# Optimization experiments

Measured on AMD Instinct MI355X. Metric: run time of the kernel, lower is better.

Reference implementation:

```python
import jax, jax.numpy as jnp
import numpy as np
from jax import lax

THRESHOLD = 10.0  # p-norm threshold in HSEM
BN_EPS = 1e-5
DN = ('NCHW', 'OIHW', 'NCHW')


def setup_inputs() -> dict:
    key = jax.random.key(0)
    ks = jax.random.split(key, 9)
    b, c, h, w = 2, 256, 64, 64
    c_out = 512
    # scale x so pairwise L2 distances straddle the threshold (dense-ish hypergraph)
    x = jax.random.normal(ks[0], (b, c, h, w), dtype=jnp.float32) * 0.4
    fc_w = jax.random.normal(ks[1], (c, c), dtype=jnp.float32) * 0.02
    fc_b = jax.random.normal(ks[2], (c,), dtype=jnp.float32) * 0.02
    bn_gamma = jnp.ones((c,), dtype=jnp.float32)
    bn_beta = jnp.zeros((c,), dtype=jnp.float32)
    down_w = jax.random.normal(ks[3], (c, c, 3, 3), dtype=jnp.float32) * 0.02
    down_b = jax.random.normal(ks[4], (c,), dtype=jnp.float32) * 0.02
    out_w = jax.random.normal(ks[5], (c_out, c, 1, 1), dtype=jnp.float32) * 0.02
    out_b = jax.random.normal(ks[6], (c_out,), dtype=jnp.float32) * 0.02
    return {"x": x, "fc_w": fc_w, "fc_b": fc_b, "bn_gamma": bn_gamma,
            "bn_beta": bn_beta, "down_w": down_w, "down_b": down_b,
            "out_w": out_w, "out_b": out_b}


def _mean_agg(path, X):
    # path: [b, n_tgt, n_src], X: [b, n_src, d]; mean aggregation with inf->0 masking
    s = jnp.sum(path, axis=2, keepdims=True)           # [b, n_tgt, 1]
    norm = jnp.where(s > 0, 1.0 / jnp.where(s > 0, s, 1.0), 0.0)
    return norm * jnp.matmul(path, X)


def reference(x, fc_w, fc_b, bn_gamma, bn_beta, down_w, down_b, out_w, out_b):
    b, c, h, w = x.shape
    n = h * w
    xf = x.reshape(b, c, n).transpose(0, 2, 1)          # [b, n, c]
    # cdist (euclidean): ||a-b|| via expansion
    sq = jnp.sum(xf * xf, axis=-1)                      # [b, n]
    d2 = sq[:, :, None] + sq[:, None, :] - 2.0 * jnp.einsum('bnc,bmc->bnm', xf, xf)
    dist = jnp.sqrt(jnp.maximum(d2, 0.0))               # [b, n, n]
    hg = (dist < THRESHOLD).astype(x.dtype)             # dynamic hypergraph incidence
    # HyPConv: fc -> v2e (H^T) -> e2v (H)
    y = jnp.einsum('bnc,dc->bnd', xf, fc_w) + fc_b      # Linear(c1, c2)
    E = _mean_agg(jnp.swapaxes(hg, 1, 2), y)            # vertex -> edge
    v = _mean_agg(hg, E)                                # edge -> vertex
    xf = v + xf                                         # residual
    x4 = xf.transpose(0, 2, 1).reshape(b, c, h, w)
    # BatchNorm2d (training-mode batch statistics, biased var)
    mean = jnp.mean(x4, axis=(0, 2, 3))
    var = jnp.var(x4, axis=(0, 2, 3))
    xn = (x4 - mean[None, :, None, None]) * lax.rsqrt(var + BN_EPS)[None, :, None, None]
    xn = xn * bn_gamma[None, :, None, None] + bn_beta[None, :, None, None]
    xa = xn * jax.nn.sigmoid(xn)                        # SiLU
    # Downsample: pad (right=1, bottom=1) then 3x3 stride-2 VALID conv
    xp = jnp.pad(xa, ((0, 0), (0, 0), (0, 1), (0, 1)))
    xd = lax.conv_general_dilated(xp, down_w, (2, 2), 'VALID', dimension_numbers=DN)
    xd = xd + down_b[None, :, None, None]
    out = lax.conv_general_dilated(xd, out_w, (1, 1), 'VALID', dimension_numbers=DN)
    out = out + out_b[None, :, None, None]
    return out
```

## Files before the change

### kernel.cpp

```cpp
#include <hip/hip_runtime.h>
#include <hip/hip_bf16.h>
#include <math.h>

#define NPIX 4096
#define CH   256

#define OFF_XP    0u
#define OFF_XR    1048576u
#define OFF_VB    2097152u
#define OFF_TBS   3145728u
#define OFF_TBS2  4194304u
#define OFF_HG    5242880u
#define OFF_SQ    6291456u
#define OFF_PART  6299648u
#define OFF_BNSS  6365184u
#define OFF_DINV  6365696u
#define OFF_W3P   6373888u
#define OFF_WFCP  6668800u
#define OFF_WOUTP 6701568u

typedef __attribute__((ext_vector_type(8))) short bf16x8;
typedef __attribute__((ext_vector_type(16))) float f32x16;

static __device__ __forceinline__ short f2b(float f) {
  __hip_bfloat16 h = __float2bfloat16(f);
  return *reinterpret_cast<short*>(&h);
}
static __device__ __forceinline__ float b2f(short s) {
  union { unsigned u; float f; } r;
  r.u = ((unsigned)(unsigned short)s) << 16;
  return r.f;
}

static __device__ __forceinline__ bf16x8 byte2bf(unsigned byte) {
  union { unsigned u[4]; bf16x8 h; } r;
  r.u[0] = ((byte * 0x8001u) & 0x10001u) * 0x3F80u;
  r.u[1] = (((byte >> 2) * 0x8001u) & 0x10001u) * 0x3F80u;
  r.u[2] = (((byte >> 4) * 0x8001u) & 0x10001u) * 0x3F80u;
  r.u[3] = (((byte >> 6) * 0x8001u) & 0x10001u) * 0x3F80u;
  return r.h;
}

static __device__ __forceinline__ size_t packoff(int m, int c) {
  return ((size_t)((m >> 5) * 16 + (c >> 4)) * 2 + ((c >> 3) & 1)) * 256 + (m & 31) * 8 + (c & 7);
}

__global__ __launch_bounds__(256) void k_front(const float* __restrict__ x,
                                               short* __restrict__ xp,
                                               float* __restrict__ sq) {
  __shared__ float lds[256][33];
  __shared__ float red2[8][32];
  const int b = blockIdx.y;
  const int n0 = blockIdx.x * 32;
  const int t = threadIdx.x;
  const float* xb = x + (size_t)b * CH * NPIX + n0;
  const int j = t & 31, cg8 = t >> 5;
#pragma unroll 4
  for (int it = 0; it < 32; ++it) {
    const int c = it * 8 + cg8;
    lds[c][j] = xb[(size_t)c * NPIX + j];
  }
  __syncthreads();
  {
    const int n = t & 31, cg = t >> 5;
    float s = 0.f;
#pragma unroll 8
    for (int i = 0; i < 32; ++i) {
      const float v = lds[cg * 32 + i][n];
      s += v * v;
    }
    red2[cg][n] = s;
  }
  short* xpb = xp + (size_t)b * NPIX * CH;
#pragma unroll
  for (int i = 0; i < 4; ++i) {
    const int f = i * 256 + t;
    const int n = f & 31, c0 = (f >> 5) * 8;
    short tmp[8];
#pragma unroll
    for (int k = 0; k < 8; ++k) tmp[k] = f2b(lds[c0 + k][n]);
    short* dst = xpb + packoff(n0 + n, c0);
    *(short4*)dst = *(short4*)&tmp[0];
    *(short4*)(dst + 4) = *(short4*)&tmp[4];
  }
  __syncthreads();
  if (t < 32) {
    float s = 0.f;
#pragma unroll
    for (int cg = 0; cg < 8; ++cg) s += red2[cg][t];
    sq[b * NPIX + n0 + t] = s;
  }
}

__global__ void k_packall(const float* __restrict__ fc_w, const float* __restrict__ ow,
                          const float* __restrict__ dw, short* __restrict__ wfcp,
                          short* __restrict__ woutp, short* __restrict__ w3p) {
  const int i = blockIdx.x * 256 + threadIdx.x;
  if (i < 65536) {
    wfcp[packoff(i >> 8, i & 255)] = f2b(fc_w[i]);
  } else if (i < 196608) {
    const int j = i - 65536;
    woutp[packoff(j >> 8, j & 255)] = f2b(ow[j]);
  } else {
    const int j = i - 196608;
    const int oc = j / 2304;
    const int rem = j % 2304;
    const int c = rem / 9, tap = rem % 9;
    const size_t off = ((size_t)((tap * 8 + (oc >> 5)) * 16 + (c >> 4)) * 2 + ((c >> 3) & 1)) * 256
                     + (oc & 31) * 8 + (c & 7);
    w3p[off] = f2b(dw[j]);
  }
}

__global__ __launch_bounds__(256, 2) void k_gram3(const short* __restrict__ xp,
                                                  const float* __restrict__ sq,
                                                  unsigned* __restrict__ hgbit) {
  const int b = blockIdx.z;
  int tt = blockIdx.x;
  int bi = 0;
  while (true) { const int cnt = 16 - (bi >> 1); if (tt < cnt) break; tt -= cnt; ++bi; }
  const int bj = (bi >> 1) + tt;
  const int i0 = bi * 128, j0 = bj * 256;

  const int t = threadIdx.x;
  const int lane = t & 63, wid = t >> 6;
  const int wm = wid >> 1, wn = wid & 1;
  const int c = lane & 31, h = lane >> 5;
  const short* xb = xp + (size_t)b * NPIX * CH;
  const int ibase = i0 + wm * 64;
  const int jbase = j0 + wn * 128;

  f32x16 acc[2][4];
#pragma unroll
  for (int m = 0; m < 2; ++m)
#pragma unroll
    for (int n = 0; n < 4; ++n)
#pragma unroll
      for (int r = 0; r < 16; ++r) acc[m][n][r] = 0.f;

  const short* pa = xb + (size_t)(ibase >> 5) * 8192 + lane * 8;
  const short* pb = xb + (size_t)(jbase >> 5) * 8192 + lane * 8;

#pragma unroll 2
  for (int kb = 0; kb < 16; ++kb) {
    const bf16x8 a0 = *(const bf16x8*)(pa + kb * 512);
    const bf16x8 a1 = *(const bf16x8*)(pa + 8192 + kb * 512);
    bf16x8 bb[4];
#pragma unroll
    for (int n = 0; n < 4; ++n) bb[n] = *(const bf16x8*)(pb + (size_t)n * 8192 + kb * 512);
#pragma unroll
    for (int n = 0; n < 4; ++n) {
      acc[0][n] = __builtin_amdgcn_mfma_f32_32x32x16_bf16(a0, bb[n], acc[0][n], 0, 0, 0);
      acc[1][n] = __builtin_amdgcn_mfma_f32_32x32x16_bf16(a1, bb[n], acc[1][n], 0, 0, 0);
    }
  }

  const int sqb = b * NPIX;
#pragma unroll
  for (int m = 0; m < 2; ++m) {
    float4 sqa[4];
#pragma unroll
    for (int q = 0; q < 4; ++q)
      sqa[q] = *(const float4*)(sq + sqb + ibase + m * 32 + q * 8 + 4 * h);
#pragma unroll
    for (int n = 0; n < 4; ++n) {
      const float sj = sq[sqb + jbase + n * 32 + c];
      const int wj = (jbase + n * 32) >> 5;
#pragma unroll
      for (int q = 0; q < 4; ++q) {
        const float sqq[4] = {sqa[q].x, sqa[q].y, sqa[q].z, sqa[q].w};
#pragma unroll
        for (int rr = 0; rr < 4; ++rr) {
          const int reg = q * 4 + rr;
          const float d2 = sqq[rr] + sj - 2.f * acc[m][n][reg];
          const unsigned long long bal = __ballot(d2 < 100.f);
          if ((lane & 31) == reg) {
            const int row = ibase + m * 32 + rr + 8 * q + 4 * h;
            const unsigned wd = h ? (unsigned)(bal >> 32) : (unsigned)bal;
            hgbit[(size_t)(sqb + row) * 128 + wj] = wd;
          }
        }
      }
    }
  }
}

__global__ void k_mirror(unsigned* __restrict__ hg) {
  const int b = blockIdx.y;
  const int g = threadIdx.x >> 5;
  const int r = threadIdx.x & 31;
  const int tile = blockIdx.x * 8 + g;
  const int ta = tile >> 7, tb = tile & 127;
  if ((ta >> 2) <= (tb >> 2)) return;
  unsigned* H = hg + (size_t)b * NPIX * 128;
  unsigned w = H[(size_t)(tb * 32 + r) * 128 + ta];
#pragma unroll
  for (int s = 16; s >= 1; s >>= 1) {
    const unsigned M = (s == 16) ? 0xFFFF0000u : (s == 8) ? 0xFF00FF00u :
                       (s == 4) ? 0xF0F0F0F0u : (s == 2) ? 0xCCCCCCCCu : 0xAAAAAAAAu;
    const unsigned p = __shfl_xor(w, s, 32);
    w = (r & s) ? ((w & M) | ((p >> s) & ~M)) : ((w & ~M) | ((p << s) & M));
  }
  H[(size_t)(ta * 32 + r) * 128 + tb] = w;
}

__global__ void k_dinv(const unsigned* __restrict__ hg, float* __restrict__ dinvf) {
  const int row = blockIdx.x, l = threadIdx.x;
  const unsigned w0 = hg[(size_t)row * 128 + l * 2];
  const unsigned w1 = hg[(size_t)row * 128 + l * 2 + 1];
  int n = __popc(w0) + __popc(w1);
#pragma unroll
  for (int off = 32; off; off >>= 1) n += __shfl_down(n, off);
  if (l == 0) dinvf[row] = 1.0f / (float)n;
}

__global__ __launch_bounds__(256) void k_mfma_fc2(const short* __restrict__ wfcp,
                                                  const short* __restrict__ xp,
                                                  short* __restrict__ C,
                                                  const float* __restrict__ bias) {
  const int b = blockIdx.z;
  xp += (size_t)b * NPIX * CH;
  C += (size_t)b << 20;
  const int t = threadIdx.x, l = t & 63, wid = t >> 6;
  const int m0 = blockIdx.y * 128 + wid * 32, n0 = blockIdx.x * 64;
  const int col = l & 31, half = l >> 5;
  f32x16 acc[2];
#pragma unroll
  for (int nt = 0; nt < 2; ++nt)
#pragma unroll
    for (int r = 0; r < 16; ++r) acc[nt][r] = 0.f;
  const short* pa = wfcp + (size_t)(m0 >> 5) * 8192 + l * 8;
  const short* pb = xp + (size_t)(n0 >> 5) * 8192 + l * 8;
#pragma unroll 4
  for (int kb = 0; kb < 16; ++kb) {
    const bf16x8 a = *(const bf16x8*)(pa + kb * 512);
    const bf16x8 b0 = *(const bf16x8*)(pb + kb * 512);
    const bf16x8 b1 = *(const bf16x8*)(pb + 8192 + kb * 512);
    acc[0] = __builtin_amdgcn_mfma_f32_32x32x16_bf16(a, b0, acc[0], 0, 0, 0);
    acc[1] = __builtin_amdgcn_mfma_f32_32x32x16_bf16(a, b1, acc[1], 0, 0, 0);
  }
  const int cb = m0 >> 5;
#pragma unroll
  for (int nt = 0; nt < 2; ++nt) {
    const int node = n0 + nt * 32 + col;
    short* dst = C + ((size_t)cb * 512 + (node >> 3)) * 256 + (node & 7);
#pragma unroll
    for (int q = 0; q < 4; ++q)
#pragma unroll
      for (int rr = 0; rr < 4; ++rr) {
        const int c31 = rr + 8 * q + 4 * half;
        dst[c31 * 8] = f2b(acc[nt][q * 4 + rr] + bias[m0 + c31]);
      }
  }
}

__global__ __launch_bounds__(256) void k_hgemm_t3(const short* __restrict__ tbs,
                                                  const unsigned* __restrict__ hg,
                                                  const float* __restrict__ dinvf,
                                                  short* __restrict__ tbs2) {
  __shared__ float red[4][64][33];
  const int b = blockIdx.z;
  const int n0 = blockIdx.x * 32;
  const int cbp = blockIdx.y;
  const int ks = threadIdx.x >> 6;
  const int l = threadIdx.x & 63;
  const int col = l & 31, half = l >> 5;
  const int sh8 = half * 8;

  f32x16 acc0, acc1;
#pragma unroll
  for (int r = 0; r < 16; ++r) { acc0[r] = 0.f; acc1[r] = 0.f; }

  const short* pa0 = tbs + ((size_t)b << 20) + ((size_t)(cbp * 2) * 512 + half) * 256
                   + col * 8 + ks * 32768;
  const short* pa1 = pa0 + 131072;
  const uint4* hrow = (const uint4*)((const unsigned char*)hg
                    + ((size_t)b * NPIX + n0 + col) * 512 + ks * 128);

#pragma unroll 2
  for (int o = 0; o < 8; ++o) {
    const uint4 wq = hrow[o];
    const unsigned ww[4] = {wq.x, wq.y, wq.z, wq.w};
#pragma unroll
    for (int s = 0; s < 4; ++s) {
      const unsigned wb = ww[s];
      const bf16x8 a00 = *(const bf16x8*)(pa0);
      const bf16x8 a01 = *(const bf16x8*)(pa0 + 512);
      const bf16x8 a10 = *(const bf16x8*)(pa1);
      const bf16x8 a11 = *(const bf16x8*)(pa1 + 512);
      pa0 += 1024; pa1 += 1024;
      const bf16x8 b0 = byte2bf((wb >> sh8) & 0xFFu);
      const bf16x8 b1 = byte2bf((wb >> (16 + sh8)) & 0xFFu);
      acc0 = __builtin_amdgcn_mfma_f32_32x32x16_bf16(a00, b0, acc0, 0, 0, 0);
      acc0 = __builtin_amdgcn_mfma_f32_32x32x16_bf16(a01, b1, acc0, 0, 0, 0);
      acc1 = __builtin_amdgcn_mfma_f32_32x32x16_bf16(a10, b0, acc1, 0, 0, 0);
      acc1 = __builtin_amdgcn_mfma_f32_32x32x16_bf16(a11, b1, acc1, 0, 0, 0);
    }
  }

#pragma unroll
  for (int r = 0; r < 16; ++r) { red[ks][l][r] = acc0[r]; red[ks][l][16 + r] = acc1[r]; }
  __syncthreads();

  const int n = n0 + col;
  const float dinv = dinvf[b * NPIX + n];
  short* dst0 = tbs2 + ((size_t)b << 20) + ((size_t)(cbp * 2) * 512 + (n >> 3)) * 256 + (n & 7);
  short* dst1 = dst0 + 131072;
#pragma unroll
  for (int rj = 0; rj < 8; ++rj) {
    const int reg = ks * 8 + rj;
    const float s = red[0][l][reg] + red[1][l][reg] + red[2][l][reg] + red[3][l][reg];
    const int rm = reg & 15;
    const int c31 = (rm & 3) + 8 * (rm >> 2) + 4 * half;
    (reg < 16 ? dst0 : dst1)[c31 * 8] = f2b(s * dinv);
  }
}

__global__ __launch_bounds__(256) void k_hgemm_n3(const unsigned* __restrict__ hg,
                                                  const short* __restrict__ tbs2,
                                                  const float* __restrict__ dinvf,
                                                  const short* __restrict__ xp,
                                                  short* __restrict__ vb) {
  __shared__ float red[4][64][33];
  const int b = blockIdx.z;
  const int cbp = blockIdx.x;
  const int m0 = blockIdx.y * 32;
  const int ks = threadIdx.x >> 6;
  const int l = threadIdx.x & 63;
  const int col = l & 31, half = l >> 5;
  const int sh8 = half * 8;

  f32x16 acc0, acc1;
#pragma unroll
  for (int r = 0; r < 16; ++r) { acc0[r] = 0.f; acc1[r] = 0.f; }

  const short* pb0 = tbs2 + ((size_t)b << 20) + ((size_t)(cbp * 2) * 512 + half) * 256
                   + col * 8 + ks * 32768;
  const short* pb1 = pb0 + 131072;
  const uint4* hrow = (const uint4*)((const unsigned char*)hg
                    + ((size_t)b * NPIX + m0 + col) * 512 + ks * 128);

#pragma unroll 2
  for (int o = 0; o < 8; ++o) {
    const uint4 wq = hrow[o];
    const unsigned ww[4] = {wq.x, wq.y, wq.z, wq.w};
#pragma unroll
    for (int s = 0; s < 4; ++s) {
      const unsigned wb = ww[s];
      const bf16x8 b00 = *(const bf16x8*)(pb0);
      const bf16x8 b01 = *(const bf16x8*)(pb0 + 512);
      const bf16x8 b10 = *(const bf16x8*)(pb1);
      const bf16x8 b11 = *(const bf16x8*)(pb1 + 512);
      pb0 += 1024; pb1 += 1024;
      const bf16x8 a0 = byte2bf((wb >> sh8) & 0xFFu);
      const bf16x8 a1 = byte2bf((wb >> (16 + sh8)) & 0xFFu);
      acc0 = __builtin_amdgcn_mfma_f32_32x32x16_bf16(a0, b00, acc0, 0, 0, 0);
      acc0 = __builtin_amdgcn_mfma_f32_32x32x16_bf16(a1, b01, acc0, 0, 0, 0);
      acc1 = __builtin_amdgcn_mfma_f32_32x32x16_bf16(a0, b10, acc1, 0, 0, 0);
      acc1 = __builtin_amdgcn_mfma_f32_32x32x16_bf16(a1, b11, acc1, 0, 0, 0);
    }
  }

#pragma unroll
  for (int r = 0; r < 16; ++r) { red[ks][l][r] = acc0[r]; red[ks][l][16 + r] = acc1[r]; }
  __syncthreads();

  const short* xpb = xp + (size_t)b * NPIX * CH;
  const int cc = cbp * 64 + col;
#pragma unroll
  for (int rj = 0; rj < 8; ++rj) {
    const int reg = ks * 8 + rj;
    const float s = red[0][l][reg] + red[1][l][reg] + red[2][l][reg] + red[3][l][reg];
    const int rm = reg & 15;
    const int r = m0 + (rm & 3) + 8 * (rm >> 2) + 4 * half;
    const int ccc = cc + (reg < 16 ? 0 : 32);
    const size_t o = ((size_t)(b * NPIX + r)) * CH + ccc;
    const short xv = xpb[packoff(r, ccc)];
    vb[o] = f2b(s * dinvf[b * NPIX + r] + b2f(xv));
  }
}

__global__ void k_bnstat(const short* __restrict__ vb, float* __restrict__ part) {
  const int t = threadIdx.x, blk = blockIdx.x;
  float s = 0.f, ss = 0.f;
  const short* p = vb + (size_t)blk * 64 * CH;
  for (int r = 0; r < 64; ++r) {
    const float v = b2f(p[r * CH + t]);
    s += v; ss += v * v;
  }
  part[blk * 512 + t] = s;
  part[blk * 512 + 256 + t] = ss;
}

__global__ void k_bnfin(const float* __restrict__ part, const float* __restrict__ gamma,
                        const float* __restrict__ beta, float* __restrict__ bnss) {
  const int t = threadIdx.x;
  float s = 0.f, ss = 0.f;
  for (int i = 0; i < 128; ++i) { s += part[i * 512 + t]; ss += part[i * 512 + 256 + t]; }
  const float mean = s * (1.f / 8192.f);
  const float var = ss * (1.f / 8192.f) - mean * mean;
  const float inv = rsqrtf(var + 1e-5f);
  const float sc = gamma[t] * inv;
  bnss[t] = sc;
  bnss[256 + t] = beta[t] - mean * sc;
}

__global__ void k_bnapply3(const short* __restrict__ vb, const float* __restrict__ bnss,
                           short* __restrict__ xpp) {
  const int i = blockIdx.x * 256 + threadIdx.x;
  const short4 sv = reinterpret_cast<const short4*>(vb)[i];
  const int c0 = (i & 63) * 4;
  const int n = (i >> 6) & 4095;
  const int b = i >> 18;
  const float4 sc = *(const float4*)(bnss + c0);
  const float4 sh = *(const float4*)(bnss + 256 + c0);
  const float u0 = b2f(sv.x) * sc.x + sh.x;
  const float u1 = b2f(sv.y) * sc.y + sh.y;
  const float u2 = b2f(sv.z) * sc.z + sh.z;
  const float u3 = b2f(sv.w) * sc.w + sh.w;
  short4 o;
  o.x = f2b(u0 / (1.f + expf(-u0)));
  o.y = f2b(u1 / (1.f + expf(-u1)));
  o.z = f2b(u2 / (1.f + expf(-u2)));
  o.w = f2b(u3 / (1.f + expf(-u3)));
  const int ih = n >> 6, iw = n & 63;
  const int p = iw & 1, ow = iw >> 1;
  const size_t off = ((size_t)(((b * 2 + p) * 64 + ih) * 16 + (c0 >> 4)) * 2 + ((c0 >> 3) & 1)) * 256
                   + ow * 8 + (c0 & 7);
  *(short4*)(xpp + off) = o;
}

__global__ __launch_bounds__(64) void k_conv5(const short* __restrict__ xpp,
                                              const short* __restrict__ w3p,
                                              float* __restrict__ convp) {
  const int ocg = blockIdx.x;
  const int oh = blockIdx.y;
  const int bz = blockIdx.z;
  const int b = bz & 1, cs = bz >> 1;
  const int l = threadIdx.x;
  const int col = l & 31;
  const bf16x8 zv = {0, 0, 0, 0, 0, 0, 0, 0};

  f32x16 acc;
#pragma unroll
  for (int r = 0; r < 16; ++r) acc[r] = 0.f;

  for (int kh = 0; kh < 3; ++kh) {
    const int ih = 2 * oh + kh;
    if (ih >= 64) continue;
#pragma unroll
    for (int kw = 0; kw < 3; ++kw) {
      const int p = kw & 1;
      const short* pa = xpp + ((size_t)((b * 2 + p) * 64 + ih) * 16 + cs * 4) * 512
                      + l * 8 + (kw == 2 ? 8 : 0);
      const short* pb = w3p + ((size_t)((kh * 3 + kw) * 8 + ocg) * 16 + cs * 4) * 512 + l * 8;
      const bool kill = (kw == 2) && (col == 31);
#pragma unroll
      for (int kb = 0; kb < 4; ++kb) {
        bf16x8 a = *(const bf16x8*)(pa + kb * 512);
        if (kill) a = zv;
        const bf16x8 bb = *(const bf16x8*)(pb + kb * 512);
        acc = __builtin_amdgcn_mfma_f32_32x32x16_bf16(a, bb, acc, 0, 0, 0);
      }
    }
  }
  const int half = l >> 5;
  const int oc = ocg * 32 + col;
#pragma unroll
  for (int q = 0; q < 4; ++q)
#pragma unroll
    for (int rr = 0; rr < 4; ++rr) {
      const int ow = rr + 8 * q + 4 * half;
      convp[((size_t)bz * 1024 + oh * 32 + ow) * 256 + oc] = acc[q * 4 + rr];
    }
}

__global__ void k_convmerge3(const float* __restrict__ convp, const float* __restrict__ db,
                             short* __restrict__ xdtb) {
  const int i = blockIdx.x * 256 + threadIdx.x;
  const int b = i >> 16, px = (i >> 6) & 1023, oc0 = (i & 63) * 4;
  const size_t base = ((size_t)px) * 256 + oc0;
  const float4 h0 = *(const float4*)(convp + ((size_t)(0 + b) << 18) + base);
  const float4 h1 = *(const float4*)(convp + ((size_t)(2 + b) << 18) + base);
  const float4 h2 = *(const float4*)(convp + ((size_t)(4 + b) << 18) + base);
  const float4 h3 = *(const float4*)(convp + ((size_t)(6 + b) << 18) + base);
  const float4 bv = *(const float4*)(db + oc0);
  short4 o;
  o.x = f2b(h0.x + h1.x + h2.x + h3.x + bv.x);
  o.y = f2b(h0.y + h1.y + h2.y + h3.y + bv.y);
  o.z = f2b(h0.z + h1.z + h2.z + h3.z + bv.z);
  o.w = f2b(h0.w + h1.w + h2.w + h3.w + bv.w);
  const size_t off = ((size_t)((b * 32 + (px >> 5)) * 16 + (oc0 >> 4)) * 2 + ((oc0 >> 3) & 1)) * 256
                   + (px & 31) * 8 + (oc0 & 7);
  *(short4*)(xdtb + off) = o;
}

__global__ __launch_bounds__(256) void k_mfma_nt2(const short* __restrict__ woutp,
                                                  const short* __restrict__ xdtb,
                                                  float* __restrict__ C,
                                                  const float* __restrict__ bias) {
  const int b = blockIdx.z;
  xdtb += (size_t)b * 1024 * CH;
  C += (size_t)b * 512 * 1024;
  const int t = threadIdx.x, l = t & 63, wid = t >> 6;
  const int m0 = blockIdx.y * 128 + wid * 32, n0 = blockIdx.x * 64;
  const int col = l & 31, half = l >> 5;
  f32x16 acc[2];
#pragma unroll
  for (int nt = 0; nt < 2; ++nt)
#pragma unroll
    for (int r = 0; r < 16; ++r) acc[nt][r] = 0.f;
  const short* pa = woutp + (size_t)(m0 >> 5) * 8192 + l * 8;
  const short* pb = xdtb + (size_t)(n0 >> 5) * 8192 + l * 8;
#pragma unroll 4
  for (int kb = 0; kb < 16; ++kb) {
    const bf16x8 a = *(const bf16x8*)(pa + kb * 512);
    const bf16x8 b0 = *(const bf16x8*)(pb + kb * 512);
    const bf16x8 b1 = *(const bf16x8*)(pb + 8192 + kb * 512);
    acc[0] = __builtin_amdgcn_mfma_f32_32x32x16_bf16(a, b0, acc[0], 0, 0, 0);
    acc[1] = __builtin_amdgcn_mfma_f32_32x32x16_bf16(a, b1, acc[1], 0, 0, 0);
  }
#pragma unroll
  for (int nt = 0; nt < 2; ++nt) {
#pragma unroll
    for (int q = 0; q < 4; ++q)
#pragma unroll
      for (int rr = 0; rr < 4; ++rr) {
        const int row = m0 + rr + 8 * q + 4 * half;
        const int cc = n0 + nt * 32 + col;
        C[(size_t)row * 1024 + cc] = acc[nt][q * 4 + rr] + bias[row];
      }
  }
}

extern "C" void kernel_launch(void* const* d_in, const int* in_sizes, int n_in,
                              void* d_out, int out_size, void* d_ws, size_t ws_size,
                              hipStream_t stream) {
  const float* x     = (const float*)d_in[0];
  const float* fc_w  = (const float*)d_in[1];
  const float* fc_b  = (const float*)d_in[2];
  const float* gamma = (const float*)d_in[3];
  const float* beta  = (const float*)d_in[4];
  const float* dw    = (const float*)d_in[5];
  const float* db    = (const float*)d_in[6];
  const float* ow    = (const float*)d_in[7];
  const float* ob    = (const float*)d_in[8];

  float* ws   = (float*)d_ws;
  short* xp   = (short*)(ws + OFF_XP);
  float* convp= ws + OFF_XP;
  short* vb   = (short*)(ws + OFF_VB);
  short* tbs  = (short*)(ws + OFF_TBS);
  short* xdtb = (short*)(ws + OFF_TBS);
  short* tbs2 = (short*)(ws + OFF_TBS2);
  short* xpp  = (short*)(ws + OFF_TBS2);
  unsigned* hg = (unsigned*)(ws + OFF_HG);
  float* sqv  = ws + OFF_SQ;
  float* part = ws + OFF_PART;
  float* bnss = ws + OFF_BNSS;
  float* dinvf= ws + OFF_DINV;
  short* w3p  = (short*)(ws + OFF_W3P);
  short* wfcp = (short*)(ws + OFF_WFCP);
  short* woutp= (short*)(ws + OFF_WOUTP);
  float* out  = (float*)d_out;

  k_front<<<dim3(128, 2), 256, 0, stream>>>(x, xp, sqv);
  k_packall<<<3072, 256, 0, stream>>>(fc_w, ow, dw, wfcp, woutp, w3p);
  k_gram3<<<dim3(272, 1, 2), 256, 0, stream>>>(xp, sqv, hg);
  k_mirror<<<dim3(2048, 2), 256, 0, stream>>>(hg);
  k_mfma_fc2<<<dim3(64, 2, 2), 256, 0, stream>>>(wfcp, xp, tbs, fc_b);
  k_dinv<<<8192, 64, 0, stream>>>(hg, dinvf);
  k_hgemm_t3<<<dim3(128, 4, 2), 256, 0, stream>>>(tbs, hg, dinvf, tbs2);
  k_hgemm_n3<<<dim3(4, 128, 2), 256, 0, stream>>>(hg, tbs2, dinvf, xp, vb);
  k_bnstat<<<128, 256, 0, stream>>>(vb, part);
  k_bnfin<<<1, 256, 0, stream>>>(part, gamma, beta, bnss);
  k_bnapply3<<<2048, 256, 0, stream>>>(vb, bnss, xpp);
  k_conv5<<<dim3(8, 32, 8), 64, 0, stream>>>(xpp, w3p, convp);
  k_convmerge3<<<512, 256, 0, stream>>>(convp, db, xdtb);
  k_mfma_nt2<<<dim3(16, 4, 2), 256, 0, stream>>>(woutp, xdtb, out, ob);
}
```

Baseline: 144.3 us.

## Double hypergraph GEMM tile size and merge small kernels to cut launches

Both hypergraph aggregation GEMMs now compute 64 rows or nodes per block instead of 32. Each block holds four accumulators, so every loaded operand fragment feeds twice as many MFMAs, halving the grid and the repeated traffic. Separately, the front transpose is merged with weight packing, and the fc GEMM with the degree-inverse kernel, so two launches are removed. The cost is more registers per thread, two extra LDS reduction and sync rounds, and half as many blocks to spread across CUs.

```diff
diff --git a/kernel.cpp b/kernel.cpp
--- a/kernel.cpp
+++ b/kernel.cpp
@@ -45,70 +45,75 @@
   return ((size_t)((m >> 5) * 16 + (c >> 4)) * 2 + ((c >> 3) & 1)) * 256 + (m & 31) * 8 + (c & 7);
 }
 
-__global__ __launch_bounds__(256) void k_front(const float* __restrict__ x,
-                                               short* __restrict__ xp,
-                                               float* __restrict__ sq) {
+__global__ __launch_bounds__(256) void k_front2(const float* __restrict__ x,
+                                                short* __restrict__ xp,
+                                                float* __restrict__ sq,
+                                                const float* __restrict__ fc_w,
+                                                const float* __restrict__ ow,
+                                                const float* __restrict__ dw,
+                                                short* __restrict__ wfcp,
+                                                short* __restrict__ woutp,
+                                                short* __restrict__ w3p) {
   __shared__ float lds[256][33];
   __shared__ float red2[8][32];
-  const int b = blockIdx.y;
-  const int n0 = blockIdx.x * 32;
+  const int bid = blockIdx.x;
   const int t = threadIdx.x;
-  const float* xb = x + (size_t)b * CH * NPIX + n0;
-  const int j = t & 31, cg8 = t >> 5;
+  if (bid < 256) {
+    const int b = bid >> 7;
+    const int n0 = (bid & 127) * 32;
+    const float* xb = x + (size_t)b * CH * NPIX + n0;
+    const int j = t & 31, cg8 = t >> 5;
 #pragma unroll 4
-  for (int it = 0; it < 32; ++it) {
-    const int c = it * 8 + cg8;
-    lds[c][j] = xb[(size_t)c * NPIX + j];
-  }
-  __syncthreads();
-  {
-    const int n = t & 31, cg = t >> 5;
-    float s = 0.f;
+    for (int it = 0; it < 32; ++it) {
+      const int c = it * 8 + cg8;
+      lds[c][j] = xb[(size_t)c * NPIX + j];
+    }
+    __syncthreads();
+    {
+      const int n = t & 31, cg = t >> 5;
+      float s = 0.f;
 #pragma unroll 8
-    for (int i = 0; i < 32; ++i) {
-      const float v = lds[cg * 32 + i][n];
-      s += v * v;
-    }
-    red2[cg][n] = s;
-  }
-  short* xpb = xp + (size_t)b * NPIX * CH;
-#pragma unroll
-  for (int i = 0; i < 4; ++i) {
-    const int f = i * 256 + t;
-    const int n = f & 31, c0 = (f >> 5) * 8;
-    short tmp[8];
-#pragma unroll
-    for (int k = 0; k < 8; ++k) tmp[k] = f2b(lds[c0 + k][n]);
-    short* dst = xpb + packoff(n0 + n, c0);
-    *(short4*)dst = *(short4*)&tmp[0];
-    *(short4*)(dst + 4) = *(short4*)&tmp[4];
-  }
-  __syncthreads();
-  if (t < 32) {
-    float s = 0.f;
-#pragma unroll
-    for (int cg = 0; cg < 8; ++cg) s += red2[cg][t];
-    sq[b * NPIX + n0 + t] = s;
-  }
-}
-
-__global__ void k_packall(const float* __restrict__ fc_w, const float* __restrict__ ow,
-                          const float* __restrict__ dw, short* __restrict__ wfcp,
-                          short* __restrict__ woutp, short* __restrict__ w3p) {
-  const int i = blockIdx.x * 256 + threadIdx.x;
-  if (i < 65536) {
-    wfcp[packoff(i >> 8, i & 255)] = f2b(fc_w[i]);
-  } else if (i < 196608) {
-    const int j = i - 65536;
-    woutp[packoff(j >> 8, j & 255)] = f2b(ow[j]);
+      for (int i = 0; i < 32; ++i) {
+        const float v = lds[cg * 32 + i][n];
+        s += v * v;
+      }
+      red2[cg][n] = s;
+    }
+    short* xpb = xp + (size_t)b * NPIX * CH;
+#pragma unroll
+    for (int i = 0; i < 4; ++i) {
+      const int f = i * 256 + t;
+      const int n = f & 31, c0 = (f >> 5) * 8;
+      short tmp[8];
+#pragma unroll
+      for (int k = 0; k < 8; ++k) tmp[k] = f2b(lds[c0 + k][n]);
+      short* dst = xpb + packoff(n0 + n, c0);
+      *(short4*)dst = *(short4*)&tmp[0];
+      *(short4*)(dst + 4) = *(short4*)&tmp[4];
+    }
+    __syncthreads();
+    if (t < 32) {
+      float s = 0.f;
+#pragma unroll
+      for (int cg = 0; cg < 8; ++cg) s += red2[cg][t];
+      sq[b * NPIX + n0 + t] = s;
+    }
   } else {
-    const int j = i - 196608;
-    const int oc = j / 2304;
-    const int rem = j % 2304;
-    const int c = rem / 9, tap = rem % 9;
-    const size_t off = ((size_t)((tap * 8 + (oc >> 5)) * 16 + (c >> 4)) * 2 + ((c >> 3) & 1)) * 256
-                     + (oc & 31) * 8 + (c & 7);
-    w3p[off] = f2b(dw[j]);
+    const int i = (bid - 256) * 256 + t;
+    if (i < 65536) {
+      wfcp[packoff(i >> 8, i & 255)] = f2b(fc_w[i]);
+    } else if (i < 196608) {
+      const int j = i - 65536;
+      woutp[packoff(j >> 8, j & 255)] = f2b(ow[j]);
+    } else {
+      const int j = i - 196608;
+      const int oc = j / 2304;
+      const int rem = j % 2304;
+      const int c = rem / 9, tap = rem % 9;
+      const size_t off = ((size_t)((tap * 8 + (oc >> 5)) * 16 + (c >> 4)) * 2 + ((c >> 3) & 1)) * 256
+                       + (oc & 31) * 8 + (c & 7);
+      w3p[off] = f2b(dw[j]);
+    }
   }
 }
 
@@ -204,25 +209,30 @@
   H[(size_t)(ta * 32 + r) * 128 + tb] = w;
 }
 
-__global__ void k_dinv(const unsigned* __restrict__ hg, float* __restrict__ dinvf) {
-  const int row = blockIdx.x, l = threadIdx.x;
-  const unsigned w0 = hg[(size_t)row * 128 + l * 2];
-  const unsigned w1 = hg[(size_t)row * 128 + l * 2 + 1];
-  int n = __popc(w0) + __popc(w1);
-#pragma unroll
-  for (int off = 32; off; off >>= 1) n += __shfl_down(n, off);
-  if (l == 0) dinvf[row] = 1.0f / (float)n;
-}
-
-__global__ __launch_bounds__(256) void k_mfma_fc2(const short* __restrict__ wfcp,
-                                                  const short* __restrict__ xp,
-                                                  short* __restrict__ C,
-                                                  const float* __restrict__ bias) {
-  const int b = blockIdx.z;
-  xp += (size_t)b * NPIX * CH;
-  C += (size_t)b << 20;
-  const int t = threadIdx.x, l = t & 63, wid = t >> 6;
-  const int m0 = blockIdx.y * 128 + wid * 32, n0 = blockIdx.x * 64;
+__global__ __launch_bounds__(256) void k_fcdinv(const short* __restrict__ wfcp,
+                                                const short* __restrict__ xp,
+                                                short* __restrict__ C,
+                                                const float* __restrict__ bias,
+                                                const unsigned* __restrict__ hg,
+                                                float* __restrict__ dinvf) {
+  const int bid = blockIdx.x;
+  const int t = threadIdx.x;
+  if (bid >= 256) {
+    const int row = (bid - 256) * 4 + (t >> 6);
+    const int l = t & 63;
+    const unsigned w0 = hg[(size_t)row * 128 + l * 2];
+    const unsigned w1 = hg[(size_t)row * 128 + l * 2 + 1];
+    int n = __popc(w0) + __popc(w1);
+#pragma unroll
+    for (int off = 32; off; off >>= 1) n += __shfl_down(n, off);
+    if (l == 0) dinvf[row] = 1.0f / (float)n;
+    return;
+  }
+  const int b = bid >> 7;
+  const short* xpb = xp + (size_t)b * NPIX * CH;
+  short* Cb = C + ((size_t)b << 20);
+  const int l = t & 63, wid = t >> 6;
+  const int m0 = ((bid >> 6) & 1) * 128 + wid * 32, n0 = (bid & 63) * 64;
   const int col = l & 31, half = l >> 5;
   f32x16 acc[2];
 #pragma unroll
@@ -230,7 +240,7 @@
 #pragma unroll
     for (int r = 0; r < 16; ++r) acc[nt][r] = 0.f;
   const short* pa = wfcp + (size_t)(m0 >> 5) * 8192 + l * 8;
-  const short* pb = xp + (size_t)(n0 >> 5) * 8192 + l * 8;
+  const short* pb = xpb + (size_t)(n0 >> 5) * 8192 + l * 8;
 #pragma unroll 4
   for (int kb = 0; kb < 16; ++kb) {
     const bf16x8 a = *(const bf16x8*)(pa + kb * 512);
@@ -243,7 +253,7 @@
 #pragma unroll
   for (int nt = 0; nt < 2; ++nt) {
     const int node = n0 + nt * 32 + col;
-    short* dst = C + ((size_t)cb * 512 + (node >> 3)) * 256 + (node & 7);
+    short* dst = Cb + ((size_t)cb * 512 + (node >> 3)) * 256 + (node & 7);
 #pragma unroll
     for (int q = 0; q < 4; ++q)
 #pragma unroll
@@ -254,69 +264,97 @@
   }
 }
 
-__global__ __launch_bounds__(256) void k_hgemm_t3(const short* __restrict__ tbs,
+__global__ __launch_bounds__(256) void k_hgemm_t4(const short* __restrict__ tbs,
                                                   const unsigned* __restrict__ hg,
                                                   const float* __restrict__ dinvf,
                                                   short* __restrict__ tbs2) {
   __shared__ float red[4][64][33];
   const int b = blockIdx.z;
-  const int n0 = blockIdx.x * 32;
+  const int n0 = blockIdx.x * 64;
   const int cbp = blockIdx.y;
   const int ks = threadIdx.x >> 6;
   const int l = threadIdx.x & 63;
   const int col = l & 31, half = l >> 5;
   const int sh8 = half * 8;
 
-  f32x16 acc0, acc1;
-#pragma unroll
-  for (int r = 0; r < 16; ++r) { acc0[r] = 0.f; acc1[r] = 0.f; }
+  f32x16 acc00, acc01, acc10, acc11;
+#pragma unroll
+  for (int r = 0; r < 16; ++r) { acc00[r] = 0.f; acc01[r] = 0.f; acc10[r] = 0.f; acc11[r] = 0.f; }
 
   const short* pa0 = tbs + ((size_t)b << 20) + ((size_t)(cbp * 2) * 512 + half) * 256
                    + col * 8 + ks * 32768;
   const short* pa1 = pa0 + 131072;
-  const uint4* hrow = (const uint4*)((const unsigned char*)hg
-                    + ((size_t)b * NPIX + n0 + col) * 512 + ks * 128);
+  const uint4* hrow0 = (const uint4*)((const unsigned char*)hg
+                     + ((size_t)b * NPIX + n0 + col) * 512 + ks * 128);
+  const uint4* hrow1 = (const uint4*)((const unsigned char*)hg
+                     + ((size_t)b * NPIX + n0 + 32 + col) * 512 + ks * 128);
 
 #pragma unroll 2
   for (int o = 0; o < 8; ++o) {
-    const uint4 wq = hrow[o];
-    const unsigned ww[4] = {wq.x, wq.y, wq.z, wq.w};
+    const uint4 wq0 = hrow0[o];
+    const uint4 wq1 = hrow1[o];
+    const unsigned ww0[4] = {wq0.x, wq0.y, wq0.z, wq0.w};
+    const unsigned ww1[4] = {wq1.x, wq1.y, wq1.z, wq1.w};
 #pragma unroll
     for (int s = 0; s < 4; ++s) {
-      const unsigned wb = ww[s];
       const bf16x8 a00 = *(const bf16x8*)(pa0);
       const bf16x8 a01 = *(const bf16x8*)(pa0 + 512);
       const bf16x8 a10 = *(const bf16x8*)(pa1);
       const bf16x8 a11 = *(const bf16x8*)(pa1 + 512);
       pa0 += 1024; pa1 += 1024;
-      const bf16x8 b0 = byte2bf((wb >> sh8) & 0xFFu);
-      const bf16x8 b1 = byte2bf((wb >> (16 + sh8)) & 0xFFu);
-      acc0 = __builtin_amdgcn_mfma_f32_32x32x16_bf16(a00, b0, acc0, 0, 0, 0);
-      acc0 = __builtin_amdgcn_mfma_f32_32x32x16_bf16(a01, b1, acc0, 0, 0, 0);
-      acc1 = __builtin_amdgcn_mfma_f32_32x32x16_bf16(a10, b0, acc1, 0, 0, 0);
-      acc1 = __builtin_amdgcn_mfma_f32_32x32x16_bf16(a11, b1, acc1, 0, 0, 0);
-    }
-  }
-
-#pragma unroll
-  for (int r = 0; r < 16; ++r) { red[ks][l][r] = acc0[r]; red[ks][l][16 + r] = acc1[r]; }
+      const bf16x8 b0 = byte2bf((ww0[s] >> sh8) & 0xFFu);
+      const bf16x8 b1 = byte2bf((ww0[s] >> (16 + sh8)) & 0xFFu);
+      const bf16x8 c0 = byte2bf((ww1[s] >> sh8) & 0xFFu);
+      const bf16x8 c1 = byte2bf((ww1[s] >> (16 + sh8)) & 0xFFu);
+      acc00 = __builtin_amdgcn_mfma_f32_32x32x16_bf16(a00, b0, acc00, 0, 0, 0);
+      acc00 = __builtin_amdgcn_mfma_f32_32x32x16_bf16(a01, b1, acc00, 0, 0, 0);
+      acc10 = __builtin_amdgcn_mfma_f32_32x32x16_bf16(a10, b0, acc10, 0, 0, 0);
+      acc10 = __builtin_amdgcn_mfma_f32_32x32x16_bf16(a11, b1, acc10, 0, 0, 0);
+      acc01 = __builtin_amdgcn_mfma_f32_32x32x16_bf16(a00, c0, acc01, 0, 0, 0);
+      acc01 = __builtin_amdgcn_mfma_f32_32x32x16_bf16(a01, c1, acc01, 0, 0, 0);
+      acc11 = __builtin_amdgcn_mfma_f32_32x32x16_bf16(a10, c0, acc11, 0, 0, 0);
+      acc11 = __builtin_amdgcn_mfma_f32_32x32x16_bf16(a11, c1, acc11, 0, 0, 0);
+    }
+  }
+
+#pragma unroll
+  for (int r = 0; r < 16; ++r) { red[ks][l][r] = acc00[r]; red[ks][l][16 + r] = acc10[r]; }
   __syncthreads();
-
-  const int n = n0 + col;
-  const float dinv = dinvf[b * NPIX + n];
-  short* dst0 = tbs2 + ((size_t)b << 20) + ((size_t)(cbp * 2) * 512 + (n >> 3)) * 256 + (n & 7);
-  short* dst1 = dst0 + 131072;
-#pragma unroll
-  for (int rj = 0; rj < 8; ++rj) {
-    const int reg = ks * 8 + rj;
-    const float s = red[0][l][reg] + red[1][l][reg] + red[2][l][reg] + red[3][l][reg];
-    const int rm = reg & 15;
-    const int c31 = (rm & 3) + 8 * (rm >> 2) + 4 * half;
-    (reg < 16 ? dst0 : dst1)[c31 * 8] = f2b(s * dinv);
-  }
-}
-
-__global__ __launch_bounds__(256) void k_hgemm_n3(const unsigned* __restrict__ hg,
+  {
+    const int n = n0 + col;
+    const float dinv = dinvf[b * NPIX + n];
+    short* dst0 = tbs2 + ((size_t)b << 20) + ((size_t)(cbp * 2) * 512 + (n >> 3)) * 256 + (n & 7);
+    short* dst1 = dst0 + 131072;
+#pragma unroll
+    for (int rj = 0; rj < 8; ++rj) {
+      const int reg = ks * 8 + rj;
+      const float s = red[0][l][reg] + red[1][l][reg] + red[2][l][reg] + red[3][l][reg];
+      const int rm = reg & 15;
+      const int c31 = (rm & 3) + 8 * (rm >> 2) + 4 * half;
+      (reg < 16 ? dst0 : dst1)[c31 * 8] = f2b(s * dinv);
+    }
+  }
+  __syncthreads();
+#pragma unroll
+  for (int r = 0; r < 16; ++r) { red[ks][l][r] = acc01[r]; red[ks][l][16 + r] = acc11[r]; }
+  __syncthreads();
+  {
+    const int n = n0 + 32 + col;
+    const float dinv = dinvf[b * NPIX + n];
+    short* dst0 = tbs2 + ((size_t)b << 20) + ((size_t)(cbp * 2) * 512 + (n >> 3)) * 256 + (n & 7);
+    short* dst1 = dst0 + 131072;
+#pragma unroll
+    for (int rj = 0; rj < 8; ++rj) {
+      const int reg = ks * 8 + rj;
+      const float s = red[0][l][reg] + red[1][l][reg] + red[2][l][reg] + red[3][l][reg];
+      const int rm = reg & 15;
+      const int c31 = (rm & 3) + 8 * (rm >> 2) + 4 * half;
+      (reg < 16 ? dst0 : dst1)[c31 * 8] = f2b(s * dinv);
+    }
+  }
+}
+
+__global__ __launch_bounds__(256) void k_hgemm_n4(const unsigned* __restrict__ hg,
                                                   const short* __restrict__ tbs2,
                                                   const float* __restrict__ dinvf,
                                                   const short* __restrict__ xp,
@@ -324,59 +362,85 @@
   __shared__ float red[4][64][33];
   const int b = blockIdx.z;
   const int cbp = blockIdx.x;
-  const int m0 = blockIdx.y * 32;
+  const int m0 = blockIdx.y * 64;
   const int ks = threadIdx.x >> 6;
   const int l = threadIdx.x & 63;
   const int col = l & 31, half = l >> 5;
   const int sh8 = half * 8;
 
-  f32x16 acc0, acc1;
-#pragma unroll
-  for (int r = 0; r < 16; ++r) { acc0[r] = 0.f; acc1[r] = 0.f; }
+  f32x16 acc00, acc01, acc10, acc11;
+#pragma unroll
+  for (int r = 0; r < 16; ++r) { acc00[r] = 0.f; acc01[r] = 0.f; acc10[r] = 0.f; acc11[r] = 0.f; }
 
   const short* pb0 = tbs2 + ((size_t)b << 20) + ((size_t)(cbp * 2) * 512 + half) * 256
                    + col * 8 + ks * 32768;
   const short* pb1 = pb0 + 131072;
-  const uint4* hrow = (const uint4*)((const unsigned char*)hg
-                    + ((size_t)b * NPIX + m0 + col) * 512 + ks * 128);
+  const uint4* hrow0 = (const uint4*)((const unsigned char*)hg
+                     + ((size_t)b * NPIX + m0 + col) * 512 + ks * 128);
+  const uint4* hrow1 = (const uint4*)((const unsigned char*)hg
+                     + ((size_t)b * NPIX + m0 + 32 + col) * 512 + ks * 128);
 
 #pragma unroll 2
   for (int o = 0; o < 8; ++o) {
-    const uint4 wq = hrow[o];
-    const unsigned ww[4] = {wq.x, wq.y, wq.z, wq.w};
+    const uint4 wq0 = hrow0[o];
+    const uint4 wq1 = hrow1[o];
+    const unsigned ww0[4] = {wq0.x, wq0.y, wq0.z, wq0.w};
+    const unsigned ww1[4] = {wq1.x, wq1.y, wq1.z, wq1.w};
 #pragma unroll
     for (int s = 0; s < 4; ++s) {
-      const unsigned wb = ww[s];
       const bf16x8 b00 = *(const bf16x8*)(pb0);
       const bf16x8 b01 = *(const bf16x8*)(pb0 + 512);
       const bf16x8 b10 = *(const bf16x8*)(pb1);
       const bf16x8 b11 = *(const bf16x8*)(pb1 + 512);
       pb0 += 1024; pb1 += 1024;
-      const bf16x8 a0 = byte2bf((wb >> sh8) & 0xFFu);
-      const bf16x8 a1 = byte2bf((wb >> (16 + sh8)) & 0xFFu);
-      acc0 = __builtin_amdgcn_mfma_f32_32x32x16_bf16(a0, b00, acc0, 0, 0, 0);
-      acc0 = __builtin_amdgcn_mfma_f32_32x32x16_bf16(a1, b01, acc0, 0, 0, 0);
-      acc1 = __builtin_amdgcn_mfma_f32_32x32x16_bf16(a0, b10, acc1, 0, 0, 0);
-      acc1 = __builtin_amdgcn_mfma_f32_32x32x16_bf16(a1, b11, acc1, 0, 0, 0);
-    }
-  }
-
-#pragma unroll
-  for (int r = 0; r < 16; ++r) { red[ks][l][r] = acc0[r]; red[ks][l][16 + r] = acc1[r]; }
+      const bf16x8 a0 = byte2bf((ww0[s] >> sh8) & 0xFFu);
+      const bf16x8 a1 = byte2bf((ww0[s] >> (16 + sh8)) & 0xFFu);
+      const bf16x8 a2 = byte2bf((ww1[s] >> sh8) & 0xFFu);
+      const bf16x8 a3 = byte2bf((ww1[s] >> (16 + sh8)) & 0xFFu);
+      acc00 = __builtin_amdgcn_mfma_f32_32x32x16_bf16(a0, b00, acc00, 0, 0, 0);
+      acc00 = __builtin_amdgcn_mfma_f32_32x32x16_bf16(a1, b01, acc00, 0, 0, 0);
+      acc01 = __builtin_amdgcn_mfma_f32_32x32x16_bf16(a0, b10, acc01, 0, 0, 0);
+      acc01 = __builtin_amdgcn_mfma_f32_32x32x16_bf16(a1, b11, acc01, 0, 0, 0);
+      acc10 = __builtin_amdgcn_mfma_f32_32x32x16_bf16(a2, b00, acc10, 0, 0, 0);
+      acc10 = __builtin_amdgcn_mfma_f32_32x32x16_bf16(a3, b01, acc10, 0, 0, 0);
+      acc11 = __builtin_amdgcn_mfma_f32_32x32x16_bf16(a2, b10, acc11, 0, 0, 0);
+      acc11 = __builtin_amdgcn_mfma_f32_32x32x16_bf16(a3, b11, acc11, 0, 0, 0);
+    }
+  }
+
+  const short* xpb = xp + (size_t)b * NPIX * CH;
+#pragma unroll
+  for (int r = 0; r < 16; ++r) { red[ks][l][r] = acc00[r]; red[ks][l][16 + r] = acc01[r]; }
   __syncthreads();
-
-  const short* xpb = xp + (size_t)b * NPIX * CH;
-  const int cc = cbp * 64 + col;
-#pragma unroll
-  for (int rj = 0; rj < 8; ++rj) {
-    const int reg = ks * 8 + rj;
-    const float s = red[0][l][reg] + red[1][l][reg] + red[2][l][reg] + red[3][l][reg];
-    const int rm = reg & 15;
-    const int r = m0 + (rm & 3) + 8 * (rm >> 2) + 4 * half;
-    const int ccc = cc + (reg < 16 ? 0 : 32);
-    const size_t o = ((size_t)(b * NPIX + r)) * CH + ccc;
-    const short xv = xpb[packoff(r, ccc)];
-    vb[o] = f2b(s * dinvf[b * NPIX + r] + b2f(xv));
+  {
+    const int cc = cbp * 64 + col;
+#pragma unroll
+    for (int rj = 0; rj < 8; ++rj) {
+      const int reg = ks * 8 + rj;
+      const float s = red[0][l][reg] + red[1][l][reg] + red[2][l][reg] + red[3][l][reg];
+      const int rm = reg & 15;
+      const int r = m0 + (rm & 3) + 8 * (rm >> 2) + 4 * half;
+      const int ccc = cc + (reg < 16 ? 0 : 32);
+      const size_t o = ((size_t)(b * NPIX + r)) * CH + ccc;
+      vb[o] = f2b(s * dinvf[b * NPIX + r] + b2f(xpb[packoff(r, ccc)]));
+    }
+  }
+  __syncthreads();
+#pragma unroll
+  for (int r = 0; r < 16; ++r) { red[ks][l][r] = acc10[r]; red[ks][l][16 + r] = acc11[r]; }
+  __syncthreads();
+  {
+    const int cc = cbp * 64 + col;
+#pragma unroll
+    for (int rj = 0; rj < 8; ++rj) {
+      const int reg = ks * 8 + rj;
+      const float s = red[0][l][reg] + red[1][l][reg] + red[2][l][reg] + red[3][l][reg];
+      const int rm = reg & 15;
+      const int r = m0 + 32 + (rm & 3) + 8 * (rm >> 2) + 4 * half;
+      const int ccc = cc + (reg < 16 ? 0 : 32);
+      const size_t o = ((size_t)(b * NPIX + r)) * CH + ccc;
+      vb[o] = f2b(s * dinvf[b * NPIX + r] + b2f(xpb[packoff(r, ccc)]));
+    }
   }
 }
 
@@ -564,14 +628,12 @@
   short* woutp= (short*)(ws + OFF_WOUTP);
   float* out  = (float*)d_out;
 
-  k_front<<<dim3(128, 2), 256, 0, stream>>>(x, xp, sqv);
-  k_packall<<<3072, 256, 0, stream>>>(fc_w, ow, dw, wfcp, woutp, w3p);
+  k_front2<<<3328, 256, 0, stream>>>(x, xp, sqv, fc_w, ow, dw, wfcp, woutp, w3p);
   k_gram3<<<dim3(272, 1, 2), 256, 0, stream>>>(xp, sqv, hg);
   k_mirror<<<dim3(2048, 2), 256, 0, stream>>>(hg);
-  k_mfma_fc2<<<dim3(64, 2, 2), 256, 0, stream>>>(wfcp, xp, tbs, fc_b);
-  k_dinv<<<8192, 64, 0, stream>>>(hg, dinvf);
-  k_hgemm_t3<<<dim3(128, 4, 2), 256, 0, stream>>>(tbs, hg, dinvf, tbs2);
-  k_hgemm_n3<<<dim3(4, 128, 2), 256, 0, stream>>>(hg, tbs2, dinvf, xp, vb);
+  k_fcdinv<<<2304, 256, 0, stream>>>(wfcp, xp, tbs, fc_b, hg, dinvf);
+  k_hgemm_t4<<<dim3(64, 4, 2), 256, 0, stream>>>(tbs, hg, dinvf, tbs2);
+  k_hgemm_n4<<<dim3(4, 64, 2), 256, 0, stream>>>(hg, tbs2, dinvf, xp, vb);
   k_bnstat<<<128, 256, 0, stream>>>(vb, part);
   k_bnfin<<<1, 256, 0, stream>>>(part, gamma, beta, bnss);
   k_bnapply3<<<2048, 256, 0, stream>>>(vb, bnss, xpp);
```

Measured after the change: 134.3 us. -6.9%, faster.
